# Kernel tuning notes

Hardware: AMD Instinct MI355X
Metric: run time of the kernel (lower is better)

## Reference

```python
import jax, jax.numpy as jnp
import numpy as np

EMBED_DIM = 1024
NUM_HEADS = 16
D_K = EMBED_DIM // NUM_HEADS
B, S = 2, 2048


def setup_inputs() -> dict:
    key = jax.random.key(0)
    kq, kk, kv = jax.random.split(key, 3)
    q = jax.random.normal(kq, (B, S, EMBED_DIM), dtype=jnp.float32)
    k = jax.random.normal(kk, (B, S, EMBED_DIM), dtype=jnp.float32)
    v = jax.random.normal(kv, (B, S, EMBED_DIM), dtype=jnp.float32)
    # causal mask, broadcast over batch and heads; 0 entries are masked out
    mask = jnp.tril(jnp.ones((S, S), dtype=jnp.int32))[None, None, :, :]
    return {"q": q, "k": k, "v": v, "mask": mask}


def _separate_heads(x):
    b, s, _ = x.shape
    return x.reshape(b, s, NUM_HEADS, D_K).transpose(0, 2, 1, 3)  # [b,h,s,d]


def reference(q, k, v, mask):
    qh = _separate_heads(q)
    kh = _separate_heads(k)
    vh = _separate_heads(v)
    # scores: [b, h, s_q, s_k]
    scores = jnp.einsum("bhqd,bhkd->bhqk", qh, kh) / jnp.sqrt(jnp.float32(D_K))
    scores = jnp.where(mask == 0, jnp.float32(-1e9), scores)
    attn = jax.nn.softmax(scores, axis=-1)  # dropout is identity in eval mode
    out = jnp.einsum("bhqk,bhkd->bhqd", attn, vh)
    out = out.transpose(0, 2, 1, 3).reshape(q.shape)
    return out, attn
```

## Files before the change

### kernel.cpp

```cpp
#include <hip/hip_runtime.h>
#include <cstdint>
#include <cstddef>


#define SLEN 2048
#define EMB  1024
#define NH   16
#define DK   64
#define BQ   128
#define BK   128

typedef __attribute__((ext_vector_type(8))) short short8;
typedef __attribute__((ext_vector_type(4))) float floatx4;
typedef __attribute__((ext_vector_type(4))) short short4v;
typedef __attribute__((ext_vector_type(2))) short short2v;

__device__ __forceinline__ short f2bf(float f) {
    union { float f; unsigned u; } c; c.f = f;
    unsigned u = c.u + 0x7fffu + ((c.u >> 16) & 1u);
    return (short)(u >> 16);
}
__device__ __forceinline__ float bf2f(short s) {
    union { unsigned u; float f; } c;
    c.u = ((unsigned)(unsigned short)s) << 16;
    return c.f;
}

#define KS_LD 72
#define VT_LD 136
#define PS_LD 136

__global__ __launch_bounds__(256, 2)
void attn_fused_kernel(const float* __restrict__ Q, const float* __restrict__ K,
                       const float* __restrict__ V, float* __restrict__ out,
                       float* __restrict__ attn)
{
    __shared__ short Ks[BK * KS_LD];
    __shared__ short Vt[DK * VT_LD];
    __shared__ short Ps[BQ * PS_LD];

    const int g   = blockIdx.x;
    const int bh  = (g >> 1) & 31;
    const int jj  = g >> 6;
    const int qt  = (g & 1) ? (15 - jj) : jj;
    const int b   = bh >> 4;
    const int h   = bh & 15;
    const int q0  = qt * BQ;

    const int t    = threadIdx.x;
    const int w    = t >> 6;
    const int lane = t & 63;
    const int quad = lane >> 4;
    const int l15  = lane & 15;

    short8 aq[2][2];
#pragma unroll
    for (int rt = 0; rt < 2; ++rt) {
        const int row = q0 + w * 32 + rt * 16 + l15;
        const float* qp = Q + (size_t)(b * SLEN + row) * EMB + h * DK;
#pragma unroll
        for (int ch = 0; ch < 2; ++ch) {
            const float4* p4 = (const float4*)(qp + ch * 32 + quad * 8);
            float4 x0 = p4[0], x1 = p4[1];
            short8 a;
            a[0] = f2bf(x0.x * 0.125f); a[1] = f2bf(x0.y * 0.125f);
            a[2] = f2bf(x0.z * 0.125f); a[3] = f2bf(x0.w * 0.125f);
            a[4] = f2bf(x1.x * 0.125f); a[5] = f2bf(x1.y * 0.125f);
            a[6] = f2bf(x1.z * 0.125f); a[7] = f2bf(x1.w * 0.125f);
            aq[rt][ch] = a;
        }
    }

    const int nk = qt + 1;

    float rs[2][4];
#pragma unroll
    for (int rt = 0; rt < 2; ++rt)
#pragma unroll
        for (int r = 0; r < 4; ++r) rs[rt][r] = 0.f;

    for (int kt = 0; kt < nk; ++kt) {
        const int k0 = kt * BK;
        __syncthreads();
        {
            const int col = (t & 15) * 4;
            const int rb  = t >> 4;
#pragma unroll
            for (int p = 0; p < 8; ++p) {
                const int row = p * 16 + rb;
                const float4 x = *(const float4*)(K + (size_t)(b * SLEN + k0 + row) * EMB + h * DK + col);
                short4v s;
                s[0] = f2bf(x.x); s[1] = f2bf(x.y); s[2] = f2bf(x.z); s[3] = f2bf(x.w);
                *(short4v*)&Ks[row * KS_LD + col] = s;
            }
        }
        __syncthreads();
        const bool diag = (kt == qt);
#pragma unroll
        for (int n = 0; n < 8; ++n) {
            const short8 b0 = *(const short8*)&Ks[(n * 16 + l15) * KS_LD + quad * 8];
            const short8 b1 = *(const short8*)&Ks[(n * 16 + l15) * KS_LD + 32 + quad * 8];
            const int colg = k0 + n * 16 + l15;
#pragma unroll
            for (int rt = 0; rt < 2; ++rt) {
                floatx4 c = {0.f, 0.f, 0.f, 0.f};
                c = __builtin_amdgcn_mfma_f32_16x16x32_bf16(aq[rt][0], b0, c, 0, 0, 0);
                c = __builtin_amdgcn_mfma_f32_16x16x32_bf16(aq[rt][1], b1, c, 0, 0, 0);
                const int rowg = q0 + w * 32 + rt * 16 + quad * 4;
#pragma unroll
                for (int r = 0; r < 4; ++r) {
                    const float p = (!diag || (colg <= rowg + r)) ? __expf(c[r]) : 0.f;
                    rs[rt][r] += p;
                }
            }
        }
    }

    float inv[2][4];
#pragma unroll
    for (int rt = 0; rt < 2; ++rt)
#pragma unroll
        for (int r = 0; r < 4; ++r) {
            float v = rs[rt][r];
            v += __shfl_xor(v, 1);
            v += __shfl_xor(v, 2);
            v += __shfl_xor(v, 4);
            v += __shfl_xor(v, 8);
            inv[rt][r] = 1.0f / v;
        }

    floatx4 o[2][4];
#pragma unroll
    for (int rt = 0; rt < 2; ++rt)
#pragma unroll
        for (int n = 0; n < 4; ++n) o[rt][n] = (floatx4){0.f, 0.f, 0.f, 0.f};

    float* const attn_bh = attn + (size_t)bh * SLEN * SLEN;

    for (int kt = 0; kt < nk; ++kt) {
        const int k0 = kt * BK;
        __syncthreads();
        {
            const int col = (t & 15) * 4;
            const int rb  = t >> 4;
#pragma unroll
            for (int p = 0; p < 8; ++p) {
                const int row = p * 16 + rb;
                const float4 x = *(const float4*)(K + (size_t)(b * SLEN + k0 + row) * EMB + h * DK + col);
                short4v s;
                s[0] = f2bf(x.x); s[1] = f2bf(x.y); s[2] = f2bf(x.z); s[3] = f2bf(x.w);
                *(short4v*)&Ks[row * KS_LD + col] = s;
            }
        }
        {
            const int kp = t & 63;
            const int dg = t >> 6;
#pragma unroll
            for (int p = 0; p < 4; ++p) {
                const int db = p * 16 + dg * 4;
                const float* vb = V + (size_t)(b * SLEN + k0 + 2 * kp) * EMB + h * DK + db;
                const float4 x0 = *(const float4*)vb;
                const float4 x1 = *(const float4*)(vb + EMB);
                short2v s;
                s[0] = f2bf(x0.x); s[1] = f2bf(x1.x); *(short2v*)&Vt[(db + 0) * VT_LD + 2 * kp] = s;
                s[0] = f2bf(x0.y); s[1] = f2bf(x1.y); *(short2v*)&Vt[(db + 1) * VT_LD + 2 * kp] = s;
                s[0] = f2bf(x0.z); s[1] = f2bf(x1.z); *(short2v*)&Vt[(db + 2) * VT_LD + 2 * kp] = s;
                s[0] = f2bf(x0.w); s[1] = f2bf(x1.w); *(short2v*)&Vt[(db + 3) * VT_LD + 2 * kp] = s;
            }
        }
        __syncthreads();
        const bool diag = (kt == qt);
#pragma unroll
        for (int n = 0; n < 8; ++n) {
            const short8 b0 = *(const short8*)&Ks[(n * 16 + l15) * KS_LD + quad * 8];
            const short8 b1 = *(const short8*)&Ks[(n * 16 + l15) * KS_LD + 32 + quad * 8];
            const int colg = k0 + n * 16 + l15;
#pragma unroll
            for (int rt = 0; rt < 2; ++rt) {
                floatx4 c = {0.f, 0.f, 0.f, 0.f};
                c = __builtin_amdgcn_mfma_f32_16x16x32_bf16(aq[rt][0], b0, c, 0, 0, 0);
                c = __builtin_amdgcn_mfma_f32_16x16x32_bf16(aq[rt][1], b1, c, 0, 0, 0);
                const int rowl = w * 32 + rt * 16 + quad * 4;
                const int rowg = q0 + rowl;
#pragma unroll
                for (int r = 0; r < 4; ++r) {
                    const float p = (!diag || (colg <= rowg + r))
                                        ? __expf(c[r]) * inv[rt][r] : 0.f;
                    Ps[(rowl + r) * PS_LD + n * 16 + l15] = f2bf(p);
                }
            }
        }
        __syncthreads();
        {
            const int c4 = (t & 31) * 4;
            const int rb = t >> 5;
#pragma unroll
            for (int i = 0; i < 16; ++i) {
                const int row = i * 8 + rb;
                const short4v pv = *(const short4v*)&Ps[row * PS_LD + c4];
                float4 f;
                f.x = bf2f(pv[0]); f.y = bf2f(pv[1]); f.z = bf2f(pv[2]); f.w = bf2f(pv[3]);
                *(float4*)(attn_bh + (size_t)(q0 + row) * SLEN + k0 + c4) = f;
            }
        }
#pragma unroll
        for (int ch = 0; ch < 4; ++ch) {
            const short8 ap0 = *(const short8*)&Ps[(w * 32 +  0 + l15) * PS_LD + ch * 32 + quad * 8];
            const short8 ap1 = *(const short8*)&Ps[(w * 32 + 16 + l15) * PS_LD + ch * 32 + quad * 8];
#pragma unroll
            for (int n = 0; n < 4; ++n) {
                const short8 bv = *(const short8*)&Vt[(n * 16 + l15) * VT_LD + ch * 32 + quad * 8];
                o[0][n] = __builtin_amdgcn_mfma_f32_16x16x32_bf16(ap0, bv, o[0][n], 0, 0, 0);
                o[1][n] = __builtin_amdgcn_mfma_f32_16x16x32_bf16(ap1, bv, o[1][n], 0, 0, 0);
            }
        }
    }

#pragma unroll
    for (int rt = 0; rt < 2; ++rt) {
        const int rowg = q0 + w * 32 + rt * 16 + quad * 4;
#pragma unroll
        for (int n = 0; n < 4; ++n) {
            const int col = h * DK + n * 16 + l15;
#pragma unroll
            for (int r = 0; r < 4; ++r)
                out[(size_t)(b * SLEN + rowg + r) * EMB + col] = o[rt][n][r];
        }
    }

    if (qt < 15) {
        const int z0 = (qt + 1) * BK;
        const float4 z = {0.f, 0.f, 0.f, 0.f};
        for (int row = w; row < BQ; row += 4) {
            float* rp = attn_bh + (size_t)(q0 + row) * SLEN;
            for (int c = z0 + lane * 4; c < SLEN; c += 256)
                *(float4*)(rp + c) = z;
        }
    }
}

extern "C" void kernel_launch(void* const* d_in, const int* in_sizes, int n_in,
                              void* d_out, int out_size, void* d_ws, size_t ws_size,
                              hipStream_t stream) {
    const float* Q = (const float*)d_in[0];
    const float* K = (const float*)d_in[1];
    const float* V = (const float*)d_in[2];
    float* out  = (float*)d_out;
    float* attn = out + (size_t)2 * SLEN * EMB;
    attn_fused_kernel<<<dim3(512), dim3(256), 0, stream>>>(Q, K, V, out, attn);
}
```

Baseline: 702.5 us.

## Split rowsum into separate kernel and pair causal query tiles per block

The row-sum pass now runs in its own kernel, which writes inverse softmax denominators to workspace. The main kernel reads them back and computes probabilities, the attn output and the PV product. Each block now handles two 64-row half tiles from mirrored query tiles (j and 15-j), so every block does the same amount of causal work, and the main kernel allows higher occupancy through smaller Ps shared memory and launch bounds. In exchange it adds a second kernel launch, extra global traffic for the denominators, and one more barrier per half-tile iteration.

Result: slower. 738.8 us (+5.2%).

```diff
diff --git a/kernel.cpp b/kernel.cpp
--- a/kernel.cpp
+++ b/kernel.cpp
@@ -5,9 +5,7 @@
 
 #define SLEN 2048
 #define EMB  1024
-#define NH   16
 #define DK   64
-#define BQ   128
 #define BK   128
 
 typedef __attribute__((ext_vector_type(8))) short short8;
@@ -30,22 +28,52 @@
 #define VT_LD 136
 #define PS_LD 136
 
-__global__ __launch_bounds__(256, 2)
-void attn_fused_kernel(const float* __restrict__ Q, const float* __restrict__ K,
-                       const float* __restrict__ V, float* __restrict__ out,
-                       float* __restrict__ attn)
+__device__ __forceinline__ void decode_block(int g, int& bh, int& j, int& half) {
+    half = g & 1;
+    j    = (g >> 1) & 7;
+    bh   = g >> 4;
+}
+
+__device__ __forceinline__ void load_q_frags(const float* __restrict__ Q, int b, int h,
+                                             int grow, int quad, short8* aq ) {
+    const float* qp = Q + (size_t)(b * SLEN + grow) * EMB + h * DK;
+#pragma unroll
+    for (int ch = 0; ch < 2; ++ch) {
+        const float4* p4 = (const float4*)(qp + ch * 32 + quad * 8);
+        float4 x0 = p4[0], x1 = p4[1];
+        short8 a;
+        a[0] = f2bf(x0.x * 0.125f); a[1] = f2bf(x0.y * 0.125f);
+        a[2] = f2bf(x0.z * 0.125f); a[3] = f2bf(x0.w * 0.125f);
+        a[4] = f2bf(x1.x * 0.125f); a[5] = f2bf(x1.y * 0.125f);
+        a[6] = f2bf(x1.z * 0.125f); a[7] = f2bf(x1.w * 0.125f);
+        aq[ch] = a;
+    }
+}
+
+__device__ __forceinline__ void stage_k(const float* __restrict__ K, int b, int h,
+                                        int k0, int t, short* Ks) {
+    const int col = (t & 15) * 4;
+    const int rb  = t >> 4;
+#pragma unroll
+    for (int p = 0; p < 8; ++p) {
+        const int row = p * 16 + rb;
+        const float4 x = *(const float4*)(K + (size_t)(b * SLEN + k0 + row) * EMB + h * DK + col);
+        short4v s;
+        s[0] = f2bf(x.x); s[1] = f2bf(x.y); s[2] = f2bf(x.z); s[3] = f2bf(x.w);
+        *(short4v*)&Ks[row * KS_LD + col] = s;
+    }
+}
+
+__global__ __launch_bounds__(256, 4)
+void rowsum_kernel(const float* __restrict__ Q, const float* __restrict__ K,
+                   float* __restrict__ invbuf)
 {
     __shared__ short Ks[BK * KS_LD];
-    __shared__ short Vt[DK * VT_LD];
-    __shared__ short Ps[BQ * PS_LD];
-
-    const int g   = blockIdx.x;
-    const int bh  = (g >> 1) & 31;
-    const int jj  = g >> 6;
-    const int qt  = (g & 1) ? (15 - jj) : jj;
-    const int b   = bh >> 4;
-    const int h   = bh & 15;
-    const int q0  = qt * BQ;
+
+    int bh, j, half; decode_block(blockIdx.x, bh, j, half);
+    const int b = bh >> 4, h = bh & 15;
+    const int qt[2]    = { j, 15 - j };
+    const int qbase[2] = { qt[0] * 128 + half * 64, qt[1] * 128 + half * 64 };
 
     const int t    = threadIdx.x;
     const int w    = t >> 6;
@@ -54,104 +82,100 @@
     const int l15  = lane & 15;
 
     short8 aq[2][2];
-#pragma unroll
-    for (int rt = 0; rt < 2; ++rt) {
-        const int row = q0 + w * 32 + rt * 16 + l15;
-        const float* qp = Q + (size_t)(b * SLEN + row) * EMB + h * DK;
-#pragma unroll
-        for (int ch = 0; ch < 2; ++ch) {
-            const float4* p4 = (const float4*)(qp + ch * 32 + quad * 8);
-            float4 x0 = p4[0], x1 = p4[1];
-            short8 a;
-            a[0] = f2bf(x0.x * 0.125f); a[1] = f2bf(x0.y * 0.125f);
-            a[2] = f2bf(x0.z * 0.125f); a[3] = f2bf(x0.w * 0.125f);
-            a[4] = f2bf(x1.x * 0.125f); a[5] = f2bf(x1.y * 0.125f);
-            a[6] = f2bf(x1.z * 0.125f); a[7] = f2bf(x1.w * 0.125f);
-            aq[rt][ch] = a;
-        }
-    }
-
-    const int nk = qt + 1;
+    load_q_frags(Q, b, h, qbase[0] + w * 16 + l15, quad, aq[0]);
+    load_q_frags(Q, b, h, qbase[1] + w * 16 + l15, quad, aq[1]);
 
     float rs[2][4];
 #pragma unroll
-    for (int rt = 0; rt < 2; ++rt)
-#pragma unroll
-        for (int r = 0; r < 4; ++r) rs[rt][r] = 0.f;
-
-    for (int kt = 0; kt < nk; ++kt) {
+    for (int qh = 0; qh < 2; ++qh)
+#pragma unroll
+        for (int r = 0; r < 4; ++r) rs[qh][r] = 0.f;
+
+    const int ktmax = 15 - j;
+    for (int kt = 0; kt <= ktmax; ++kt) {
         const int k0 = kt * BK;
         __syncthreads();
-        {
-            const int col = (t & 15) * 4;
-            const int rb  = t >> 4;
-#pragma unroll
-            for (int p = 0; p < 8; ++p) {
-                const int row = p * 16 + rb;
-                const float4 x = *(const float4*)(K + (size_t)(b * SLEN + k0 + row) * EMB + h * DK + col);
-                short4v s;
-                s[0] = f2bf(x.x); s[1] = f2bf(x.y); s[2] = f2bf(x.z); s[3] = f2bf(x.w);
-                *(short4v*)&Ks[row * KS_LD + col] = s;
-            }
-        }
+        stage_k(K, b, h, k0, t, Ks);
         __syncthreads();
-        const bool diag = (kt == qt);
 #pragma unroll
         for (int n = 0; n < 8; ++n) {
             const short8 b0 = *(const short8*)&Ks[(n * 16 + l15) * KS_LD + quad * 8];
             const short8 b1 = *(const short8*)&Ks[(n * 16 + l15) * KS_LD + 32 + quad * 8];
             const int colg = k0 + n * 16 + l15;
 #pragma unroll
-            for (int rt = 0; rt < 2; ++rt) {
+            for (int qh = 0; qh < 2; ++qh) {
+                if (qh == 0 && kt > j) continue;
                 floatx4 c = {0.f, 0.f, 0.f, 0.f};
-                c = __builtin_amdgcn_mfma_f32_16x16x32_bf16(aq[rt][0], b0, c, 0, 0, 0);
-                c = __builtin_amdgcn_mfma_f32_16x16x32_bf16(aq[rt][1], b1, c, 0, 0, 0);
-                const int rowg = q0 + w * 32 + rt * 16 + quad * 4;
+                c = __builtin_amdgcn_mfma_f32_16x16x32_bf16(aq[qh][0], b0, c, 0, 0, 0);
+                c = __builtin_amdgcn_mfma_f32_16x16x32_bf16(aq[qh][1], b1, c, 0, 0, 0);
+                const int rowg = qbase[qh] + w * 16 + quad * 4;
+                const bool diag = (kt == qt[qh]);
 #pragma unroll
                 for (int r = 0; r < 4; ++r) {
                     const float p = (!diag || (colg <= rowg + r)) ? __expf(c[r]) : 0.f;
-                    rs[rt][r] += p;
-                }
-            }
-        }
-    }
-
-    float inv[2][4];
-#pragma unroll
-    for (int rt = 0; rt < 2; ++rt)
+                    rs[qh][r] += p;
+                }
+            }
+        }
+    }
+
+#pragma unroll
+    for (int qh = 0; qh < 2; ++qh)
 #pragma unroll
         for (int r = 0; r < 4; ++r) {
-            float v = rs[rt][r];
+            float v = rs[qh][r];
             v += __shfl_xor(v, 1);
             v += __shfl_xor(v, 2);
             v += __shfl_xor(v, 4);
             v += __shfl_xor(v, 8);
-            inv[rt][r] = 1.0f / v;
-        }
+            if (l15 == 0)
+                invbuf[(size_t)bh * SLEN + qbase[qh] + w * 16 + quad * 4 + r] = 1.0f / v;
+        }
+}
+
+__global__ __launch_bounds__(256, 3)
+void attn_main_kernel(const float* __restrict__ Q, const float* __restrict__ K,
+                      const float* __restrict__ V, const float* __restrict__ invbuf,
+                      float* __restrict__ out, float* __restrict__ attn)
+{
+    __shared__ short Ks[BK * KS_LD];
+    __shared__ short Vt[DK * VT_LD];
+    __shared__ short Ps[64 * PS_LD];
+
+    int bh, j, half; decode_block(blockIdx.x, bh, j, half);
+    const int b = bh >> 4, h = bh & 15;
+    const int qt[2]    = { j, 15 - j };
+    const int qbase[2] = { qt[0] * 128 + half * 64, qt[1] * 128 + half * 64 };
+
+    const int t    = threadIdx.x;
+    const int w    = t >> 6;
+    const int lane = t & 63;
+    const int quad = lane >> 4;
+    const int l15  = lane & 15;
+
+    short8 aq[2][2];
+    load_q_frags(Q, b, h, qbase[0] + w * 16 + l15, quad, aq[0]);
+    load_q_frags(Q, b, h, qbase[1] + w * 16 + l15, quad, aq[1]);
+
+    float invr[2][4];
+#pragma unroll
+    for (int qh = 0; qh < 2; ++qh)
+#pragma unroll
+        for (int r = 0; r < 4; ++r)
+            invr[qh][r] = invbuf[(size_t)bh * SLEN + qbase[qh] + w * 16 + quad * 4 + r];
 
     floatx4 o[2][4];
 #pragma unroll
-    for (int rt = 0; rt < 2; ++rt)
-#pragma unroll
-        for (int n = 0; n < 4; ++n) o[rt][n] = (floatx4){0.f, 0.f, 0.f, 0.f};
+    for (int qh = 0; qh < 2; ++qh)
+#pragma unroll
+        for (int n = 0; n < 4; ++n) o[qh][n] = (floatx4){0.f, 0.f, 0.f, 0.f};
 
     float* const attn_bh = attn + (size_t)bh * SLEN * SLEN;
 
-    for (int kt = 0; kt < nk; ++kt) {
+    const int ktmax = 15 - j;
+    for (int kt = 0; kt <= ktmax; ++kt) {
         const int k0 = kt * BK;
-        __syncthreads();
-        {
-            const int col = (t & 15) * 4;
-            const int rb  = t >> 4;
-#pragma unroll
-            for (int p = 0; p < 8; ++p) {
-                const int row = p * 16 + rb;
-                const float4 x = *(const float4*)(K + (size_t)(b * SLEN + k0 + row) * EMB + h * DK + col);
-                short4v s;
-                s[0] = f2bf(x.x); s[1] = f2bf(x.y); s[2] = f2bf(x.z); s[3] = f2bf(x.w);
-                *(short4v*)&Ks[row * KS_LD + col] = s;
-            }
-        }
+        stage_k(K, b, h, k0, t, Ks);
         {
             const int kp = t & 63;
             const int dg = t >> 6;
@@ -169,70 +193,73 @@
             }
         }
         __syncthreads();
-        const bool diag = (kt == qt);
-#pragma unroll
-        for (int n = 0; n < 8; ++n) {
-            const short8 b0 = *(const short8*)&Ks[(n * 16 + l15) * KS_LD + quad * 8];
-            const short8 b1 = *(const short8*)&Ks[(n * 16 + l15) * KS_LD + 32 + quad * 8];
-            const int colg = k0 + n * 16 + l15;
-#pragma unroll
-            for (int rt = 0; rt < 2; ++rt) {
+
+#pragma unroll
+        for (int qh = 0; qh < 2; ++qh) {
+            if (qh == 0 && kt > j) continue;
+            const bool diag = (kt == qt[qh]);
+#pragma unroll
+            for (int n = 0; n < 8; ++n) {
+                const short8 b0 = *(const short8*)&Ks[(n * 16 + l15) * KS_LD + quad * 8];
+                const short8 b1 = *(const short8*)&Ks[(n * 16 + l15) * KS_LD + 32 + quad * 8];
+                const int colg = k0 + n * 16 + l15;
                 floatx4 c = {0.f, 0.f, 0.f, 0.f};
-                c = __builtin_amdgcn_mfma_f32_16x16x32_bf16(aq[rt][0], b0, c, 0, 0, 0);
-                c = __builtin_amdgcn_mfma_f32_16x16x32_bf16(aq[rt][1], b1, c, 0, 0, 0);
-                const int rowl = w * 32 + rt * 16 + quad * 4;
-                const int rowg = q0 + rowl;
+                c = __builtin_amdgcn_mfma_f32_16x16x32_bf16(aq[qh][0], b0, c, 0, 0, 0);
+                c = __builtin_amdgcn_mfma_f32_16x16x32_bf16(aq[qh][1], b1, c, 0, 0, 0);
+                const int rowl = w * 16 + quad * 4;
+                const int rowg = qbase[qh] + rowl;
 #pragma unroll
                 for (int r = 0; r < 4; ++r) {
                     const float p = (!diag || (colg <= rowg + r))
-                                        ? __expf(c[r]) * inv[rt][r] : 0.f;
+                                        ? __expf(c[r]) * invr[qh][r] : 0.f;
                     Ps[(rowl + r) * PS_LD + n * 16 + l15] = f2bf(p);
                 }
             }
-        }
-        __syncthreads();
-        {
-            const int c4 = (t & 31) * 4;
-            const int rb = t >> 5;
-#pragma unroll
-            for (int i = 0; i < 16; ++i) {
-                const int row = i * 8 + rb;
-                const short4v pv = *(const short4v*)&Ps[row * PS_LD + c4];
-                float4 f;
-                f.x = bf2f(pv[0]); f.y = bf2f(pv[1]); f.z = bf2f(pv[2]); f.w = bf2f(pv[3]);
-                *(float4*)(attn_bh + (size_t)(q0 + row) * SLEN + k0 + c4) = f;
-            }
-        }
-#pragma unroll
-        for (int ch = 0; ch < 4; ++ch) {
-            const short8 ap0 = *(const short8*)&Ps[(w * 32 +  0 + l15) * PS_LD + ch * 32 + quad * 8];
-            const short8 ap1 = *(const short8*)&Ps[(w * 32 + 16 + l15) * PS_LD + ch * 32 + quad * 8];
-#pragma unroll
-            for (int n = 0; n < 4; ++n) {
-                const short8 bv = *(const short8*)&Vt[(n * 16 + l15) * VT_LD + ch * 32 + quad * 8];
-                o[0][n] = __builtin_amdgcn_mfma_f32_16x16x32_bf16(ap0, bv, o[0][n], 0, 0, 0);
-                o[1][n] = __builtin_amdgcn_mfma_f32_16x16x32_bf16(ap1, bv, o[1][n], 0, 0, 0);
-            }
-        }
-    }
-
-#pragma unroll
-    for (int rt = 0; rt < 2; ++rt) {
-        const int rowg = q0 + w * 32 + rt * 16 + quad * 4;
+            __syncthreads();
+            {
+                const int c4 = (t & 31) * 4;
+                const int rb = t >> 5;
+#pragma unroll
+                for (int i = 0; i < 8; ++i) {
+                    const int row = i * 8 + rb;
+                    const short4v pv = *(const short4v*)&Ps[row * PS_LD + c4];
+                    float4 f;
+                    f.x = bf2f(pv[0]); f.y = bf2f(pv[1]); f.z = bf2f(pv[2]); f.w = bf2f(pv[3]);
+                    *(float4*)(attn_bh + (size_t)(qbase[qh] + row) * SLEN + k0 + c4) = f;
+                }
+            }
+#pragma unroll
+            for (int ch = 0; ch < 4; ++ch) {
+                const short8 ap = *(const short8*)&Ps[(w * 16 + l15) * PS_LD + ch * 32 + quad * 8];
+#pragma unroll
+                for (int n = 0; n < 4; ++n) {
+                    const short8 bv = *(const short8*)&Vt[(n * 16 + l15) * VT_LD + ch * 32 + quad * 8];
+                    o[qh][n] = __builtin_amdgcn_mfma_f32_16x16x32_bf16(ap, bv, o[qh][n], 0, 0, 0);
+                }
+            }
+            __syncthreads();
+        }
+    }
+
+#pragma unroll
+    for (int qh = 0; qh < 2; ++qh) {
+        const int rowg = qbase[qh] + w * 16 + quad * 4;
 #pragma unroll
         for (int n = 0; n < 4; ++n) {
             const int col = h * DK + n * 16 + l15;
 #pragma unroll
             for (int r = 0; r < 4; ++r)
-                out[(size_t)(b * SLEN + rowg + r) * EMB + col] = o[rt][n][r];
-        }
-    }
-
-    if (qt < 15) {
-        const int z0 = (qt + 1) * BK;
-        const float4 z = {0.f, 0.f, 0.f, 0.f};
-        for (int row = w; row < BQ; row += 4) {
-            float* rp = attn_bh + (size_t)(q0 + row) * SLEN;
+                out[(size_t)(b * SLEN + rowg + r) * EMB + col] = o[qh][n][r];
+        }
+    }
+
+    const float4 z = {0.f, 0.f, 0.f, 0.f};
+#pragma unroll
+    for (int qh = 0; qh < 2; ++qh) {
+        const int z0 = (qt[qh] + 1) * BK;
+        if (z0 >= SLEN) continue;
+        for (int row = w; row < 64; row += 4) {
+            float* rp = attn_bh + (size_t)(qbase[qh] + row) * SLEN;
             for (int c = z0 + lane * 4; c < SLEN; c += 256)
                 *(float4*)(rp + c) = z;
         }
@@ -245,7 +272,10 @@
     const float* Q = (const float*)d_in[0];
     const float* K = (const float*)d_in[1];
     const float* V = (const float*)d_in[2];
-    float* out  = (float*)d_out;
-    float* attn = out + (size_t)2 * SLEN * EMB;
-    attn_fused_kernel<<<dim3(512), dim3(256), 0, stream>>>(Q, K, V, out, attn);
-}
+    float* out    = (float*)d_out;
+    float* attn   = out + (size_t)2 * SLEN * EMB;
+    float* invbuf = (float*)d_ws;
+
+    rowsum_kernel<<<dim3(512), dim3(256), 0, stream>>>(Q, K, invbuf);
+    attn_main_kernel<<<dim3(512), dim3(256), 0, stream>>>(Q, K, V, invbuf, out, attn);
+}
```
